# Optimization experiments

Measured on AMD Instinct MI355X. Metric: run time of the kernel, lower is better.

The kernel has to match this reference:

```python
import jax, jax.numpy as jnp
from jax import lax
import numpy as np

CHANNEL_N = 16
EMB = 128
B, H, W = 16, 256, 256


def setup_inputs() -> dict:
    key = jax.random.key(0)
    ks = jax.random.split(key, 8)
    x = jax.random.uniform(ks[0], (B, CHANNEL_N, H, W), dtype=jnp.float32)
    fire_mask = (jax.random.uniform(ks[1], (B, 1, H, W)) < 0.5).astype(jnp.float32)
    s = 0.05
    w1 = jax.random.normal(ks[2], (3 * CHANNEL_N, EMB), dtype=jnp.float32) * s
    b1 = jnp.zeros((EMB,), jnp.float32)
    w2 = jax.random.normal(ks[3], (EMB, EMB), dtype=jnp.float32) * s
    b2 = jnp.zeros((EMB,), jnp.float32)
    w3 = jax.random.normal(ks[4], (EMB, CHANNEL_N), dtype=jnp.float32) * s
    b3 = jnp.zeros((CHANNEL_N,), jnp.float32)
    return {"x": x, "fire_mask": fire_mask, "w1": w1, "b1": b1, "w2": w2, "b2": b2, "w3": w3, "b3": b3}


def _forward(x, fire_mask, w1, b1, w2, b2, w3, b3):
    # depthwise Sobel conv (torch conv2d = cross-correlation, same as lax default)
    sob = jnp.array([[-1., 0., 1.], [-2., 0., 2.], [-1., 0., 1.]], jnp.float32)
    kx = jnp.tile(sob[None, None], (CHANNEL_N, 1, 1, 1))   # OIHW, groups=16
    ky = jnp.tile(sob.T[None, None], (CHANNEL_N, 1, 1, 1))
    conv = lambda k: lax.conv_general_dilated(x, k, (1, 1), 'SAME', feature_group_count=CHANNEL_N)
    feats = jnp.concatenate([x, conv(kx), conv(ky)], axis=1)  # [B,48,H,W]

    # alive mask: 3x3 max-pool of alpha channel > 0.1
    alpha = x[:, 3:4]
    pooled = lax.reduce_window(alpha, -jnp.inf, lax.max, (1, 1, 3, 3), (1, 1, 1, 1), 'SAME')
    alive = (pooled > 0.1).astype(x.dtype)
    combined = fire_mask * alive                     # [B,1,H,W]
    # nonzero-indexing semantics: update written wherever combined != 0
    sel = (combined != 0).astype(x.dtype)

    f = feats.transpose(0, 2, 3, 1)                  # [B,H,W,48]
    h = jax.nn.relu(f @ w1 + b1)
    h = jax.nn.relu(h @ w2 + b2)
    u = h @ w3 + b3                                  # [B,H,W,16]
    updates = u * sel.transpose(0, 2, 3, 1)          # zero outside selected cells
    return updates.transpose(0, 3, 1, 2)             # [B,16,H,W]


def reference(x, fire_mask, w1, b1, w2, b2, w3, b3):
    return _forward(x, fire_mask, w1, b1, w2, b2, w3, b3)
```

## Files before the change

kernel.cpp:

```cpp
#include <hip/hip_runtime.h>


#define NPX (1u << 20)

using bf16x8 = __attribute__((ext_vector_type(8))) __bf16;
using f32x4  = __attribute__((ext_vector_type(4))) float;

__device__ __forceinline__ unsigned f2bf(float f) {
    unsigned u = __float_as_uint(f);
    u += 0x7fffu + ((u >> 16) & 1u);
    return u >> 16;
}

#define WS1_OFF 0
#define WS2_OFF 8192
#define WS3_OFF 24576

__global__ __launch_bounds__(1024)
void prep_weights(const float* __restrict__ w1, const float* __restrict__ w2,
                  const float* __restrict__ w3, unsigned short* __restrict__ ws) {
    const int s = threadIdx.x;
    {
        const int mt = s >> 7, kb = (s >> 6) & 1, lane = s & 63;
        const int q = lane >> 4, ln = lane & 15;
#pragma unroll
        for (int j = 0; j < 8; ++j) {
            const int k = kb * 32 + q * 8 + j;
            float val = 0.f;
            if (k < 48) { const int c = k / 3, t = k - 3 * c; val = w1[(t * 16 + c) * 128 + mt * 16 + ln]; }
            ws[WS1_OFF + s * 8 + j] = (unsigned short)f2bf(val);
        }
    }
    for (int s2 = s; s2 < 2048; s2 += 1024) {
        const int mt = s2 >> 8, kb = (s2 >> 6) & 3, lane = s2 & 63;
        const int q = lane >> 4, ln = lane & 15;
#pragma unroll
        for (int j = 0; j < 8; ++j) {
            const int k = kb * 32 + q * 8 + j;
            ws[WS2_OFF + s2 * 8 + j] = (unsigned short)f2bf(w2[k * 128 + mt * 16 + ln]);
        }
    }
    if (s < 256) {
        const int kb = s >> 6, lane = s & 63;
        const int q = lane >> 4, ln = lane & 15;
#pragma unroll
        for (int j = 0; j < 8; ++j) {
            const int k = kb * 32 + q * 8 + j;
            ws[WS3_OFF + s * 8 + j] = (unsigned short)f2bf(w3[k * 16 + ln]);
        }
    }
}

#define XS_W 260

#define SM_XS     0
#define SM_FEATS  49920
#define SM_SEL    78592
#define SM_W2     79616
#define SM_H      112384
#define SM_OBUF   145152
#define SM_TOTAL  161792

#define H_SWZ(j, ln) ((((j) ^ ((ln) & 7)) << 4))

extern "C" __global__ __launch_bounds__(256, 1)
void fused_kernel(const float* __restrict__ x, const float* __restrict__ fmask,
                  const unsigned short* __restrict__ wf,
                  const float* __restrict__ b1, const float* __restrict__ b2,
                  const float* __restrict__ b3, float* __restrict__ out) {
    extern __shared__ char smem[];
    float (*xs)[16][XS_W] = (float (*)[16][XS_W])(smem + SM_XS);
    unsigned short* featsL = (unsigned short*)(smem + SM_FEATS);
    float* selL = (float*)(smem + SM_SEL);
    char* W2L = smem + SM_W2;

    const int t = threadIdx.x;
    const int wv = t >> 6, lane = t & 63;
    const int q = lane >> 4, ln = lane & 15;
    char* Ha = smem + SM_H + wv * 8192;
    char* Hb = Ha + 4096;
    float* OB = (float*)(smem + SM_OBUF + wv * 4160);

    const int bb = blockIdx.x >> 5;
    const int h0 = (blockIdx.x & 31) << 3;
    const float* xb = x + ((size_t)bb << 20);

    {
        const uint4* src = (const uint4*)(wf + WS2_OFF);
        uint4* dst = (uint4*)W2L;
#pragma unroll
        for (int i = 0; i < 8; ++i) dst[t + i * 256] = src[t + i * 256];
    }
    bf16x8 W1f[8][2], W3f[4];
#pragma unroll
    for (int mt = 0; mt < 8; ++mt) {
        W1f[mt][0] = *(const bf16x8*)(wf + WS1_OFF + ((mt * 2 + 0) * 64 + lane) * 8);
        W1f[mt][1] = *(const bf16x8*)(wf + WS1_OFF + ((mt * 2 + 1) * 64 + lane) * 8);
    }
#pragma unroll
    for (int kb = 0; kb < 4; ++kb)
        W3f[kb] = *(const bf16x8*)(wf + WS3_OFF + (kb * 64 + lane) * 8);

    const int col = t;
    const int cL = (col > 0)   ? col - 1 : 0;
    const int cR = (col < 255) ? col + 1 : 255;
    const float mL = (col > 0)   ? 1.f : 0.f;
    const float mR = (col < 255) ? 1.f : 0.f;

    float4 stg[4];
#define STAGE_ISSUE(r2) do { _Pragma("unroll")                                   \
    for (int i = 0; i < 4; ++i) {                                                \
        const int idx = t + i * 256;                                             \
        const int ch = idx >> 6; const int c4 = (idx & 63) << 2;                 \
        float4 v = make_float4(0.f, 0.f, 0.f, 0.f);                              \
        if ((unsigned)(r2) < 256u)                                               \
            v = *(const float4*)(xb + ((size_t)ch << 16) + (r2) * 256 + c4);     \
        stg[i] = v; } } while (0)
#define STAGE_STORE(slot) do { _Pragma("unroll")                                 \
    for (int i = 0; i < 4; ++i) {                                                \
        const int idx = t + i * 256;                                             \
        const int ch = idx >> 6; const int c4 = (idx & 63) << 2;                 \
        *(float4*)&xs[slot][ch][c4] = stg[i]; } } while (0)

    STAGE_ISSUE(h0 - 1); STAGE_STORE((h0 + 2) % 3);
    STAGE_ISSUE(h0);     STAGE_STORE(h0 % 3);
    STAGE_ISSUE(h0 + 1);

    for (int rr = 0; rr < 8; ++rr) {
        const int r = h0 + rr;
        STAGE_STORE((r + 1) % 3);
        __syncthreads();
        if (rr < 7) STAGE_ISSUE(r + 2);
        const float fv = fmask[((size_t)bb << 16) + r * 256 + col];

        const int sT = (r + 2) % 3, sC = r % 3, sB = (r + 1) % 3;
        unsigned pk[24];
        unsigned carry = 0;
        float selv = 0.f;
#pragma unroll
        for (int c = 0; c < 16; ++c) {
            const float* rT = xs[sT][c];
            const float* rC = xs[sC][c];
            const float* rB = xs[sB][c];
            const float v00 = rT[cL] * mL, v01 = rT[col], v02 = rT[cR] * mR;
            const float v10 = rC[cL] * mL, v11 = rC[col], v12 = rC[cR] * mR;
            const float v20 = rB[cL] * mL, v21 = rB[col], v22 = rB[cR] * mR;
            const float sx = (v02 + 2.f * v12 + v22) - (v00 + 2.f * v10 + v20);
            const float sy = (v20 + 2.f * v21 + v22) - (v00 + 2.f * v01 + v02);
            if (c == 3) {
                float mx = fmaxf(fmaxf(fmaxf(v00, v01), fmaxf(v02, v10)),
                                 fmaxf(fmaxf(v11, v12), fmaxf(fmaxf(v20, v21), v22)));
                selv = (mx > 0.1f) ? 1.f : 0.f;
            }
            const unsigned ux = f2bf(v11), usx = f2bf(sx), usy = f2bf(sy);
            if ((c & 1) == 0) { pk[(c >> 1) * 3] = ux | (usx << 16); carry = usy; }
            else { pk[(c >> 1) * 3 + 1] = carry | (ux << 16);
                   pk[(c >> 1) * 3 + 2] = usx | (usy << 16); }
        }
        selL[col] = (fv != 0.f) ? selv : 0.f;
        {
            uint4* dstf = (uint4*)(featsL + col * 56);
#pragma unroll
            for (int j = 0; j < 6; ++j)
                dstf[j] = make_uint4(pk[j * 4 + 0], pk[j * 4 + 1], pk[j * 4 + 2], pk[j * 4 + 3]);
        }
        __syncthreads();

#pragma unroll
        for (int sub = 0; sub < 4; ++sub) {
            char* H = (sub & 1) ? Hb : Ha;
            const int pxl = wv * 64 + sub * 16 + ln;
            const unsigned short* fp = featsL + pxl * 56;
            const bf16x8 Bk0 = *(const bf16x8*)(fp + q * 8);
            bf16x8 Bk1 = {};
            if (q < 2) Bk1 = *(const bf16x8*)(fp + 32 + q * 8);
#pragma unroll
            for (int mt = 0; mt < 8; ++mt) {
                f32x4 acc = *(const f32x4*)(b1 + mt * 16 + q * 4);
                acc = __builtin_amdgcn_mfma_f32_16x16x32_bf16(W1f[mt][0], Bk0, acc, 0, 0, 0);
                acc = __builtin_amdgcn_mfma_f32_16x16x32_bf16(W1f[mt][1], Bk1, acc, 0, 0, 0);
                const unsigned r01 = f2bf(fmaxf(acc[0], 0.f)) | (f2bf(fmaxf(acc[1], 0.f)) << 16);
                const unsigned r23 = f2bf(fmaxf(acc[2], 0.f)) | (f2bf(fmaxf(acc[3], 0.f)) << 16);
                *(uint2*)(H + ln * 256 + H_SWZ(mt * 2 + (q >> 1), ln) + ((q & 1) << 3))
                    = make_uint2(r01, r23);
            }
            bf16x8 B2[4];
#pragma unroll
            for (int kb = 0; kb < 4; ++kb)
                B2[kb] = *(const bf16x8*)(H + ln * 256 + H_SWZ(kb * 4 + q, ln));
#pragma unroll
            for (int mt = 0; mt < 8; ++mt) {
                f32x4 acc = *(const f32x4*)(b2 + mt * 16 + q * 4);
#pragma unroll
                for (int kb = 0; kb < 4; ++kb) {
                    const bf16x8 Af = *(const bf16x8*)(W2L + ((mt * 4 + kb) * 64 + lane) * 16);
                    acc = __builtin_amdgcn_mfma_f32_16x16x32_bf16(Af, B2[kb], acc, 0, 0, 0);
                }
                const unsigned r01 = f2bf(fmaxf(acc[0], 0.f)) | (f2bf(fmaxf(acc[1], 0.f)) << 16);
                const unsigned r23 = f2bf(fmaxf(acc[2], 0.f)) | (f2bf(fmaxf(acc[3], 0.f)) << 16);
                *(uint2*)(H + ln * 256 + H_SWZ(mt * 2 + (q >> 1), ln) + ((q & 1) << 3))
                    = make_uint2(r01, r23);
            }
            f32x4 acc3 = *(const f32x4*)(b3 + q * 4);
#pragma unroll
            for (int kb = 0; kb < 4; ++kb) {
                const bf16x8 B3 = *(const bf16x8*)(H + ln * 256 + H_SWZ(kb * 4 + q, ln));
                acc3 = __builtin_amdgcn_mfma_f32_16x16x32_bf16(W3f[kb], B3, acc3, 0, 0, 0);
            }
            const float sv = selL[pxl];
#pragma unroll
            for (int r4 = 0; r4 < 4; ++r4)
                OB[(q * 4 + r4) * 65 + sub * 16 + ln] = acc3[r4] * sv;
        }
        {
            float* orow = out + (((size_t)bb * 16) << 16) + (size_t)r * 256 + wv * 64 + lane;
#pragma unroll
            for (int ch = 0; ch < 16; ++ch)
                orow[(size_t)ch << 16] = OB[ch * 65 + lane];
        }
    }
#undef STAGE_ISSUE
#undef STAGE_STORE
}

extern "C" void kernel_launch(void* const* d_in, const int* in_sizes, int n_in,
                              void* d_out, int out_size, void* d_ws, size_t ws_size,
                              hipStream_t stream) {
    (void)in_sizes; (void)n_in; (void)out_size; (void)ws_size;
    const float* x  = (const float*)d_in[0];
    const float* fm = (const float*)d_in[1];
    const float* w1 = (const float*)d_in[2];
    const float* b1 = (const float*)d_in[3];
    const float* w2 = (const float*)d_in[4];
    const float* b2 = (const float*)d_in[5];
    const float* w3 = (const float*)d_in[6];
    const float* b3 = (const float*)d_in[7];
    float* o = (float*)d_out;
    unsigned short* ws = (unsigned short*)d_ws;

    prep_weights<<<dim3(1), dim3(1024), 0, stream>>>(w1, w2, w3, ws);

    hipFuncSetAttribute((const void*)fused_kernel,
                        hipFuncAttributeMaxDynamicSharedMemorySize, SM_TOTAL);
    fused_kernel<<<dim3(512), dim3(256), SM_TOTAL, stream>>>(x, fm, ws, b1, b2, b3, o);
}
```

Measured before the change: 254.1 us.

## Interleave two pixel tiles per MLP pass and stage biases in LDS

The MLP loop now handles two 16-pixel tiles at once, so independent MFMA chains can interleave and each W2 fragment read from LDS serves both tiles. Biases move into shared memory, and the per-wave output buffer is dropped in favour of reusing the H scratch as a bounce buffer, with each 32-pixel half written out separately. The weight-prep kernel is split across 13 blocks of 256 threads instead of one 1024-thread block. The cost is higher register pressure from the doubled accumulators and fragments, plus smaller and more frequent output store groups.

```diff
diff --git a/kernel.cpp b/kernel.cpp
--- a/kernel.cpp
+++ b/kernel.cpp
@@ -16,11 +16,12 @@
 #define WS2_OFF 8192
 #define WS3_OFF 24576
 
-__global__ __launch_bounds__(1024)
+__global__ __launch_bounds__(256)
 void prep_weights(const float* __restrict__ w1, const float* __restrict__ w2,
                   const float* __restrict__ w3, unsigned short* __restrict__ ws) {
-    const int s = threadIdx.x;
-    {
+    const int gid = blockIdx.x * 256 + threadIdx.x;
+    if (gid < 1024) {
+        const int s = gid;
         const int mt = s >> 7, kb = (s >> 6) & 1, lane = s & 63;
         const int q = lane >> 4, ln = lane & 15;
 #pragma unroll
@@ -30,8 +31,8 @@
             if (k < 48) { const int c = k / 3, t = k - 3 * c; val = w1[(t * 16 + c) * 128 + mt * 16 + ln]; }
             ws[WS1_OFF + s * 8 + j] = (unsigned short)f2bf(val);
         }
-    }
-    for (int s2 = s; s2 < 2048; s2 += 1024) {
+    } else if (gid < 3072) {
+        const int s2 = gid - 1024;
         const int mt = s2 >> 8, kb = (s2 >> 6) & 3, lane = s2 & 63;
         const int q = lane >> 4, ln = lane & 15;
 #pragma unroll
@@ -39,14 +40,14 @@
             const int k = kb * 32 + q * 8 + j;
             ws[WS2_OFF + s2 * 8 + j] = (unsigned short)f2bf(w2[k * 128 + mt * 16 + ln]);
         }
-    }
-    if (s < 256) {
-        const int kb = s >> 6, lane = s & 63;
+    } else if (gid < 3328) {
+        const int s3 = gid - 3072;
+        const int kb = s3 >> 6, lane = s3 & 63;
         const int q = lane >> 4, ln = lane & 15;
 #pragma unroll
         for (int j = 0; j < 8; ++j) {
             const int k = kb * 32 + q * 8 + j;
-            ws[WS3_OFF + s * 8 + j] = (unsigned short)f2bf(w3[k * 16 + ln]);
+            ws[WS3_OFF + s3 * 8 + j] = (unsigned short)f2bf(w3[k * 16 + ln]);
         }
     }
 }
@@ -58,8 +59,8 @@
 #define SM_SEL    78592
 #define SM_W2     79616
 #define SM_H      112384
-#define SM_OBUF   145152
-#define SM_TOTAL  161792
+#define SM_BIAS   145152
+#define SM_TOTAL  146240
 
 #define H_SWZ(j, ln) ((((j) ^ ((ln) & 7)) << 4))
 
@@ -73,13 +74,13 @@
     unsigned short* featsL = (unsigned short*)(smem + SM_FEATS);
     float* selL = (float*)(smem + SM_SEL);
     char* W2L = smem + SM_W2;
+    float* biasL = (float*)(smem + SM_BIAS);
 
     const int t = threadIdx.x;
     const int wv = t >> 6, lane = t & 63;
     const int q = lane >> 4, ln = lane & 15;
     char* Ha = smem + SM_H + wv * 8192;
     char* Hb = Ha + 4096;
-    float* OB = (float*)(smem + SM_OBUF + wv * 4160);
 
     const int bb = blockIdx.x >> 5;
     const int h0 = (blockIdx.x & 31) << 3;
@@ -90,6 +91,8 @@
         uint4* dst = (uint4*)W2L;
 #pragma unroll
         for (int i = 0; i < 8; ++i) dst[t + i * 256] = src[t + i * 256];
+        biasL[t] = (t < 128) ? b1[t] : b2[t - 128];
+        if (t < 16) biasL[256 + t] = b3[t];
     }
     bf16x8 W1f[8][2], W3f[4];
 #pragma unroll
@@ -167,56 +170,86 @@
         __syncthreads();
 
 #pragma unroll
-        for (int sub = 0; sub < 4; ++sub) {
-            char* H = (sub & 1) ? Hb : Ha;
-            const int pxl = wv * 64 + sub * 16 + ln;
-            const unsigned short* fp = featsL + pxl * 56;
-            const bf16x8 Bk0 = *(const bf16x8*)(fp + q * 8);
-            bf16x8 Bk1 = {};
-            if (q < 2) Bk1 = *(const bf16x8*)(fp + 32 + q * 8);
+        for (int p = 0; p < 2; ++p) {
+            const int pxA = wv * 64 + p * 32 + ln;
+            const int pxB = pxA + 16;
+            const unsigned short* fpA = featsL + pxA * 56;
+            const unsigned short* fpB = featsL + pxB * 56;
+            const bf16x8 BkA0 = *(const bf16x8*)(fpA + q * 8);
+            const bf16x8 BkB0 = *(const bf16x8*)(fpB + q * 8);
+            bf16x8 BkA1 = {}, BkB1 = {};
+            if (q < 2) {
+                BkA1 = *(const bf16x8*)(fpA + 32 + q * 8);
+                BkB1 = *(const bf16x8*)(fpB + 32 + q * 8);
+            }
 #pragma unroll
             for (int mt = 0; mt < 8; ++mt) {
-                f32x4 acc = *(const f32x4*)(b1 + mt * 16 + q * 4);
-                acc = __builtin_amdgcn_mfma_f32_16x16x32_bf16(W1f[mt][0], Bk0, acc, 0, 0, 0);
-                acc = __builtin_amdgcn_mfma_f32_16x16x32_bf16(W1f[mt][1], Bk1, acc, 0, 0, 0);
-                const unsigned r01 = f2bf(fmaxf(acc[0], 0.f)) | (f2bf(fmaxf(acc[1], 0.f)) << 16);
-                const unsigned r23 = f2bf(fmaxf(acc[2], 0.f)) | (f2bf(fmaxf(acc[3], 0.f)) << 16);
-                *(uint2*)(H + ln * 256 + H_SWZ(mt * 2 + (q >> 1), ln) + ((q & 1) << 3))
-                    = make_uint2(r01, r23);
-            }
-            bf16x8 B2[4];
-#pragma unroll
-            for (int kb = 0; kb < 4; ++kb)
-                B2[kb] = *(const bf16x8*)(H + ln * 256 + H_SWZ(kb * 4 + q, ln));
+                const f32x4 bz = *(const f32x4*)(biasL + mt * 16 + q * 4);
+                f32x4 aA = bz, aB = bz;
+                aA = __builtin_amdgcn_mfma_f32_16x16x32_bf16(W1f[mt][0], BkA0, aA, 0, 0, 0);
+                aB = __builtin_amdgcn_mfma_f32_16x16x32_bf16(W1f[mt][0], BkB0, aB, 0, 0, 0);
+                aA = __builtin_amdgcn_mfma_f32_16x16x32_bf16(W1f[mt][1], BkA1, aA, 0, 0, 0);
+                aB = __builtin_amdgcn_mfma_f32_16x16x32_bf16(W1f[mt][1], BkB1, aB, 0, 0, 0);
+                const unsigned a01 = f2bf(fmaxf(aA[0], 0.f)) | (f2bf(fmaxf(aA[1], 0.f)) << 16);
+                const unsigned a23 = f2bf(fmaxf(aA[2], 0.f)) | (f2bf(fmaxf(aA[3], 0.f)) << 16);
+                const unsigned b01 = f2bf(fmaxf(aB[0], 0.f)) | (f2bf(fmaxf(aB[1], 0.f)) << 16);
+                const unsigned b23 = f2bf(fmaxf(aB[2], 0.f)) | (f2bf(fmaxf(aB[3], 0.f)) << 16);
+                const int off = ln * 256 + H_SWZ(mt * 2 + (q >> 1), ln) + ((q & 1) << 3);
+                *(uint2*)(Ha + off) = make_uint2(a01, a23);
+                *(uint2*)(Hb + off) = make_uint2(b01, b23);
+            }
+            bf16x8 B2A[4], B2B[4];
+#pragma unroll
+            for (int kb = 0; kb < 4; ++kb) {
+                const int off = ln * 256 + H_SWZ(kb * 4 + q, ln);
+                B2A[kb] = *(const bf16x8*)(Ha + off);
+                B2B[kb] = *(const bf16x8*)(Hb + off);
+            }
 #pragma unroll
             for (int mt = 0; mt < 8; ++mt) {
-                f32x4 acc = *(const f32x4*)(b2 + mt * 16 + q * 4);
+                const f32x4 bz = *(const f32x4*)(biasL + 128 + mt * 16 + q * 4);
+                f32x4 aA = bz, aB = bz;
 #pragma unroll
                 for (int kb = 0; kb < 4; ++kb) {
                     const bf16x8 Af = *(const bf16x8*)(W2L + ((mt * 4 + kb) * 64 + lane) * 16);
-                    acc = __builtin_amdgcn_mfma_f32_16x16x32_bf16(Af, B2[kb], acc, 0, 0, 0);
+                    aA = __builtin_amdgcn_mfma_f32_16x16x32_bf16(Af, B2A[kb], aA, 0, 0, 0);
+                    aB = __builtin_amdgcn_mfma_f32_16x16x32_bf16(Af, B2B[kb], aB, 0, 0, 0);
                 }
-                const unsigned r01 = f2bf(fmaxf(acc[0], 0.f)) | (f2bf(fmaxf(acc[1], 0.f)) << 16);
-                const unsigned r23 = f2bf(fmaxf(acc[2], 0.f)) | (f2bf(fmaxf(acc[3], 0.f)) << 16);
-                *(uint2*)(H + ln * 256 + H_SWZ(mt * 2 + (q >> 1), ln) + ((q & 1) << 3))
-                    = make_uint2(r01, r23);
-            }
-            f32x4 acc3 = *(const f32x4*)(b3 + q * 4);
+                const unsigned a01 = f2bf(fmaxf(aA[0], 0.f)) | (f2bf(fmaxf(aA[1], 0.f)) << 16);
+                const unsigned a23 = f2bf(fmaxf(aA[2], 0.f)) | (f2bf(fmaxf(aA[3], 0.f)) << 16);
+                const unsigned b01 = f2bf(fmaxf(aB[0], 0.f)) | (f2bf(fmaxf(aB[1], 0.f)) << 16);
+                const unsigned b23 = f2bf(fmaxf(aB[2], 0.f)) | (f2bf(fmaxf(aB[3], 0.f)) << 16);
+                const int off = ln * 256 + H_SWZ(mt * 2 + (q >> 1), ln) + ((q & 1) << 3);
+                *(uint2*)(Ha + off) = make_uint2(a01, a23);
+                *(uint2*)(Hb + off) = make_uint2(b01, b23);
+            }
+            const f32x4 bz3 = *(const f32x4*)(biasL + 256 + q * 4);
+            f32x4 a3A = bz3, a3B = bz3;
 #pragma unroll
             for (int kb = 0; kb < 4; ++kb) {
-                const bf16x8 B3 = *(const bf16x8*)(H + ln * 256 + H_SWZ(kb * 4 + q, ln));
-                acc3 = __builtin_amdgcn_mfma_f32_16x16x32_bf16(W3f[kb], B3, acc3, 0, 0, 0);
-            }
-            const float sv = selL[pxl];
-#pragma unroll
-            for (int r4 = 0; r4 < 4; ++r4)
-                OB[(q * 4 + r4) * 65 + sub * 16 + ln] = acc3[r4] * sv;
-        }
-        {
-            float* orow = out + (((size_t)bb * 16) << 16) + (size_t)r * 256 + wv * 64 + lane;
-#pragma unroll
-            for (int ch = 0; ch < 16; ++ch)
-                orow[(size_t)ch << 16] = OB[ch * 65 + lane];
+                const int off = ln * 256 + H_SWZ(kb * 4 + q, ln);
+                const bf16x8 B3A = *(const bf16x8*)(Ha + off);
+                const bf16x8 B3B = *(const bf16x8*)(Hb + off);
+                a3A = __builtin_amdgcn_mfma_f32_16x16x32_bf16(W3f[kb], B3A, a3A, 0, 0, 0);
+                a3B = __builtin_amdgcn_mfma_f32_16x16x32_bf16(W3f[kb], B3B, a3B, 0, 0, 0);
+            }
+            const float svA = selL[pxA];
+            const float svB = selL[pxB];
+            float* bounce = (float*)Ha;
+#pragma unroll
+            for (int r4 = 0; r4 < 4; ++r4) {
+                bounce[(q * 4 + r4) * 34 + ln]      = a3A[r4] * svA;
+                bounce[(q * 4 + r4) * 34 + 16 + ln] = a3B[r4] * svB;
+            }
+            const int px32 = lane & 31;
+            const int chb  = lane >> 5;
+            float* orow = out + (((size_t)(bb * 16)) << 16) + (size_t)r * 256
+                        + wv * 64 + p * 32 + px32;
+#pragma unroll
+            for (int i = 0; i < 8; ++i) {
+                const int ch = chb + 2 * i;
+                orow[(size_t)ch << 16] = bounce[ch * 34 + px32];
+            }
         }
     }
 #undef STAGE_ISSUE
@@ -238,7 +271,7 @@
     float* o = (float*)d_out;
     unsigned short* ws = (unsigned short*)d_ws;
 
-    prep_weights<<<dim3(1), dim3(1024), 0, stream>>>(w1, w2, w3, ws);
+    prep_weights<<<dim3(13), dim3(256), 0, stream>>>(w1, w2, w3, ws);
 
     hipFuncSetAttribute((const void*)fused_kernel,
                         hipFuncAttributeMaxDynamicSharedMemorySize, SM_TOTAL);
```

Measured after the change: 267.5 us. 1.05x slower.
